# Kernel tuning notes

Measured on AMD Instinct MI355X. Metric: run time of the kernel, lower is better.

Reference implementation:

```python
import jax, jax.numpy as jnp
import numpy as np


def rosa_batch(bits):
    """Vectorized ROSA (suffix-automaton 'predict next symbol of longest previously
    seen suffix') for a batch of binary sequences.

    bits: [N, T] int32 in {0,1}. Returns [N, T] int32 in {-1, 0, 1}.

    Equivalent to the serial suffix-automaton: at step i, let L = max_{j<i}
    lcs(i, j) (longest common suffix of prefixes ending at i and j). If L == 0
    the answer is -1; otherwise let e = max{ j < i : lcs(i, j) == L } (most
    recent occurrence end, matching the automaton's last-endpos bookkeeping)
    and the answer is bits[e + 1]. lcs follows the standard recurrence
    lcs(i, j) = (x[i] == x[j]) * (lcs(i-1, j-1) + 1), computed with a scan
    over i carrying the length-T lcs row, vmapped implicitly over N.
    """
    N, T = bits.shape
    jpos = jnp.arange(T)

    def step(prev, it):
        i, xt = it  # i: scalar step index, xt: [N] current symbols
        # prev[:, j] = lcs(i-1, j); shift to get lcs(i-1, j-1)
        shifted = jnp.concatenate([jnp.zeros((N, 1), prev.dtype), prev[:, :-1]], axis=1)
        cur = jnp.where(bits == xt[:, None], shifted + 1, 0)  # [N, T] lcs(i, j)
        valid = jpos[None, :] < i
        cm = jnp.where(valid, cur, -1)
        L = cm.max(axis=1)  # [N] longest previously-seen suffix length
        # most recent j < i achieving the max
        e = jnp.where(valid & (cm == L[:, None]), jpos[None, :], -1).max(axis=1)
        nxt = jnp.take_along_axis(bits, jnp.clip(e + 1, 0, T - 1)[:, None], axis=1)[:, 0]
        y = jnp.where(L > 0, nxt, -1)
        return cur, y

    _, ys = jax.lax.scan(step, jnp.zeros((N, T), jnp.int32), (jnp.arange(T), bits.T))
    return ys.T


def rosa_bits_btc(bits_btc):
    """bits_btc: [B, T, C] -> idx [B, T, C]; ROSA runs along T per (b, c)."""
    B, T, C = bits_btc.shape
    seqs = bits_btc.transpose(0, 2, 1).reshape(B * C, T)
    return rosa_batch(seqs).reshape(B, C, T).transpose(0, 2, 1)


def setup_inputs() -> dict:
    key = jax.random.key(0)
    B, T, C = 4, 2048, 128
    x = jax.random.normal(key, (B, T, C), dtype=jnp.float32)
    emb0 = jnp.full((1, 1, C), -1e-5, dtype=jnp.float32)
    emb1 = jnp.full((1, 1, C), 1e-5, dtype=jnp.float32)
    return {"x": x, "emb0": emb0, "emb1": emb1}


def reference(x, emb0, emb1):
    bits = (x > 0).astype(jnp.int32)
    idx = rosa_bits_btc(bits)  # [B, T, C] in {-1, 0, 1}
    return jnp.where(idx == -1, jnp.zeros_like(x), jnp.where(idx == 1, emb1, emb0))
```

## Files before the change

kernel.cpp:

```cpp
#include <hip/hip_runtime.h>


#define TT 2048
#define CC 128
#define NW 64
#define NSEQ 512
#define SBITS_WORDS (NSEQ * NW)
#define RES_WORDS (NSEQ * TT)

typedef short          s16x2 __attribute__((ext_vector_type(2)));
typedef unsigned short u16x2 __attribute__((ext_vector_type(2)));

__device__ __forceinline__ unsigned pk_sign(unsigned x) {
    s16x2 v = __builtin_bit_cast(s16x2, x);
    v = v >> 15;
    return __builtin_bit_cast(unsigned, v);
}
__device__ __forceinline__ unsigned pk_shl1(unsigned x) {
    u16x2 v = __builtin_bit_cast(u16x2, x);
    v = v << 1;
    return __builtin_bit_cast(unsigned, v);
}
__device__ __forceinline__ unsigned pk_addsat64(unsigned x) {
    u16x2 v = __builtin_bit_cast(u16x2, x);
    u16x2 c = {64, 64};
    v = __builtin_elementwise_add_sat(v, c);
    return __builtin_bit_cast(unsigned, v);
}
__device__ __forceinline__ unsigned pk_maxu(unsigned a, unsigned b) {
    u16x2 x = __builtin_bit_cast(u16x2, a);
    u16x2 y = __builtin_bit_cast(u16x2, b);
    u16x2 r = __builtin_elementwise_max(x, y);
    return __builtin_bit_cast(unsigned, r);
}

__global__ void k_bits(const float* __restrict__ x, unsigned* __restrict__ sbits)
{
    const int b = blockIdx.x >> 6;
    const int w = blockIdx.x & 63;
    const int t = threadIdx.x;
    __shared__ unsigned char sbyt[32 * 132];

    #pragma unroll
    for (int r = 0; r < 16; ++r) {
        const int e  = t + (r << 8);
        const int ii = e >> 7;
        const int c  = e & 127;
        const float v = x[((size_t)(b * TT + (w << 5) + ii)) * CC + c];
        sbyt[ii * 132 + c] = (v > 0.0f) ? 1u : 0u;
    }
    __syncthreads();

    if (t < CC) {
        unsigned word = 0u;
        #pragma unroll
        for (int ii = 0; ii < 32; ++ii)
            word |= (unsigned)(sbyt[ii * 132 + t] & 1u) << ii;
        sbits[((b << 7) | t) * NW + w] = word;
    }
}

__global__ __launch_bounds__(256, 4) void k_dp2(
    const unsigned* __restrict__ sbits, unsigned* __restrict__ res)
{
    const int u = blockIdx.x;
    const int q = blockIdx.y;
    int k = 0;
    #pragma unroll
    for (int kk = 1; kk < 8; ++kk) if (u >= (kk * (kk + 1)) / 2) k = kk;
    const int chunk = u - (k * (k + 1)) / 2;
    const int D0 = 1 + (chunk << 8);

    const int tid  = threadIdx.x;
    const int lane = tid & 63;
    const int wv   = tid >> 6;
    const int g    = lane >> 3;
    const int lm   = lane & 7;
    const int wB   = k << 3;
    const int wloc = wB + lm;
    const int kb   = k << 8;

    __shared__ unsigned pad[128];
    __shared__ unsigned seedl[256];
    __shared__ unsigned wres[4][8][33];

    if (tid < 64) pad[tid] = 0u;
    else if (tid < 128) pad[tid] = sbits[q * NW + (tid - 64)];
    __syncthreads();

    {
        const int d = D0 + tid;
        unsigned acc = 0u;
        if (d < kb) {
            const int dw = d >> 5, dr = d & 31;
            for (int w = wB - 1; w >= 0; --w) {
                const int sw = w - dw;
                const unsigned u0 = pad[64 + sw];
                const unsigned u1 = pad[63 + sw];
                const unsigned shw = dr ? ((u0 << dr) | (u1 >> (32 - dr))) : u0;
                const unsigned ew = (sw > 0) ? 0xFFFFFFFFu
                                  : ((sw == 0) ? (0xFFFFFFFFu << dr) : 0u);
                const unsigned mw = (~(pad[64 + w] ^ shw)) & ew;
                const unsigned t2 = (mw == 0xFFFFFFFFu) ? 32u
                                  : (unsigned)__builtin_clz(~mw);
                acc += t2;
                if (t2 < 32u) break;
            }
        }
        seedl[tid] = acc;
    }
    __syncthreads();

    const unsigned a = pad[64 + wloc];

    unsigned lmaxp[16];
    #pragma unroll
    for (int j = 0; j < 16; ++j) lmaxp[j] = 0u;

    unsigned incs[8];

    #pragma unroll
    for (int it = 0; it < 8; ++it) {
        const int d  = D0 + (it << 5) + (wv << 3) + g;
        const int dw = d >> 5;
        const int dr = d & 31;

        const int s = wloc - dw;
        const unsigned b0 = pad[64 + s];
        const unsigned b1 = pad[63 + s];
        const unsigned sh = dr ? ((b0 << dr) | (b1 >> (32 - dr))) : b0;
        const unsigned em = (s > 0) ? 0xFFFFFFFFu
                          : ((s == 0) ? (0xFFFFFFFFu << dr) : 0u);
        const unsigned m = (~(a ^ sh)) & em;

        const unsigned seedv = seedl[(it << 5) + (wv << 3) + g];
        const unsigned pm = (unsigned)__shfl_up((int)m, 1, 64);
        const unsigned lead = (unsigned)__builtin_clz(~pm | 1u);
        unsigned inc = (lm == 0) ? seedv : lead;

        if (__builtin_expect(
                __ballot((lm > 0) && (pm == 0xFFFFFFFFu)) != 0ULL, 0)) {
            if ((lm > 0) && (pm == 0xFFFFFFFFu)) {
                unsigned acc = 0u;
                int w;
                for (w = wloc - 1; w >= wB; --w) {
                    const int sw = w - dw;
                    const unsigned u0 = pad[64 + sw];
                    const unsigned u1 = pad[63 + sw];
                    const unsigned shw = dr ? ((u0 << dr) | (u1 >> (32 - dr))) : u0;
                    const unsigned ew = (sw > 0) ? 0xFFFFFFFFu
                                      : ((sw == 0) ? (0xFFFFFFFFu << dr) : 0u);
                    const unsigned mw = (~(pad[64 + w] ^ shw)) & ew;
                    const unsigned t2 = (mw == 0xFFFFFFFFu) ? 32u
                                      : (unsigned)__builtin_clz(~mw);
                    acc += t2;
                    if (t2 < 32u) break;
                }
                if (w < wB) acc += seedv;
                inc = acc;
            }
        }
        incs[it] = inc;

        const unsigned nm   = ~m;
        const unsigned u16c = (unsigned)__builtin_clz((nm << 16) | 0x8000u);
        const unsigned s16  = u16c + ((u16c == 16u) ? inc : 0u);

        const unsigned itcv = (unsigned)((7 - it) << 3) * 0x10001u;
        const unsigned ci = inc > 1023u ? 1023u : inc;
        const unsigned cs = s16 > 1023u ? 1023u : s16;
        unsigned rp = (ci << 6) | (cs << 22) | itcv;

        const unsigned mr  = __builtin_bitreverse32(m);
        unsigned mmr = (mr >> 16) | (mr << 16);

        #pragma unroll
        for (int j = 0; j < 16; ++j) {
            const unsigned sm = pk_sign(mmr);
            mmr = pk_shl1(mmr);
            rp  = pk_addsat64(rp);
            rp  = (rp & sm) | (itcv & ~sm);
            lmaxp[j] = pk_maxu(lmaxp[j], rp);
        }
    }

    const unsigned gk2 = (unsigned)(7 - g) * 0x10001u;
    #pragma unroll
    for (int j = 0; j < 16; ++j) lmaxp[j] |= gk2;

    #pragma unroll
    for (int j = 0; j < 16; ++j) {
        unsigned v = lmaxp[j];
        v = pk_maxu(v, (unsigned)__shfl_xor((int)v, 8, 64));
        v = pk_maxu(v, (unsigned)__shfl_xor((int)v, 16, 64));
        v = pk_maxu(v, (unsigned)__shfl_xor((int)v, 32, 64));
        lmaxp[j] = v;
    }

    unsigned mx = lmaxp[0];
    #pragma unroll
    for (int j = 1; j < 16; ++j) mx = pk_maxu(mx, lmaxp[j]);
    const bool ovf = ((mx & 0x0000FC00u) == 0x0000FC00u) ||
                     ((mx & 0xFC000000u) == 0xFC000000u);

    if (__builtin_expect(__ballot(ovf) == 0ULL, 1)) {
        const unsigned Kw = 2048u - (unsigned)D0 - (unsigned)(wv << 3) - 231u;
        #pragma unroll
        for (int e = 0; e < 4; ++e) {
            const int j = ((g & 3) << 2) + e;
            const unsigned r32 = lmaxp[j];
            const unsigned h = (g >= 4) ? (r32 >> 16) : (r32 & 0xFFFFu);
            const unsigned v = ((h >> 6) << 11) + ((h & 0x38u) << 2) + (h & 7u) + Kw;
            wres[wv][lm][(g << 2) + e] = v;
        }
    } else {
        unsigned lm32[32];
        #pragma unroll
        for (int bb = 0; bb < 32; ++bb) lm32[bb] = 0u;
        for (int it = 0; it < 8; ++it) {
            const int d  = D0 + (it << 5) + (wv << 3) + g;
            const int dw = d >> 5;
            const int dr = d & 31;
            const unsigned dcode = (unsigned)(TT - d) & 2047u;
            const int s = wloc - dw;
            const unsigned b0 = pad[64 + s];
            const unsigned b1 = pad[63 + s];
            const unsigned sh = dr ? ((b0 << dr) | (b1 >> (32 - dr))) : b0;
            const unsigned em = (s > 0) ? 0xFFFFFFFFu
                              : ((s == 0) ? (0xFFFFFFFFu << dr) : 0u);
            const unsigned m = (~(a ^ sh)) & em;
            unsigned pkv = (incs[it] << 11) | dcode;
            for (int bb = 0; bb < 32; ++bb) {
                pkv = ((m >> bb) & 1u) ? (pkv + 0x800u) : dcode;
                lm32[bb] = lm32[bb] >= pkv ? lm32[bb] : pkv;
            }
        }
        #pragma unroll
        for (int bb = 0; bb < 32; ++bb) {
            unsigned v = lm32[bb];
            v = max(v, (unsigned)__shfl_xor((int)v, 8, 64));
            v = max(v, (unsigned)__shfl_xor((int)v, 16, 64));
            v = max(v, (unsigned)__shfl_xor((int)v, 32, 64));
            lm32[bb] = v;
        }
        if (g == 0) {
            #pragma unroll
            for (int bb = 0; bb < 32; ++bb) wres[wv][lm][bb] = lm32[bb];
        }
    }
    __syncthreads();

    {
        const int lw = tid >> 5, bb = tid & 31;
        const unsigned v = max(max(wres[0][lw][bb], wres[1][lw][bb]),
                               max(wres[2][lw][bb], wres[3][lw][bb]));
        if (v >> 11) {
            const int i = ((wB + lw) << 5) + bb;
            atomicMax(&res[(size_t)q * TT + i], v);
        }
    }
}

__global__ void k_dec(const unsigned* __restrict__ sbits,
                      const unsigned* __restrict__ res,
                      const float* __restrict__ emb0,
                      const float* __restrict__ emb1,
                      float* __restrict__ out)
{
    const int b  = blockIdx.y;
    const int i0 = blockIdx.x << 4;
    const int t  = threadIdx.x;
    __shared__ float trans[16][CC + 4];

    const int c  = t >> 1;
    const int q8 = (t & 1) << 3;
    const unsigned* rp = res + ((size_t)((b << 7) | c) * TT) + i0 + q8;
    const unsigned* bw = sbits + ((size_t)((b << 7) | c)) * NW;
    const float e0 = emb0[c], e1 = emb1[c];

    #pragma unroll
    for (int jj = 0; jj < 8; ++jj) {
        const unsigned v = rp[jj];
        const int i = i0 + q8 + jj;
        float val = 0.0f;
        if (v >> 11) {
            const int d   = TT - (int)(v & 2047u);
            const int e1p = i - d + 1;
            val = ((bw[e1p >> 5] >> (e1p & 31)) & 1u) ? e1 : e0;
        }
        trans[q8 + jj][c] = val;
    }
    __syncthreads();

    const int ii = t >> 4;
    const int c0 = (t & 15) << 3;
    float4 w0 = *(const float4*)&trans[ii][c0];
    float4 w1 = *(const float4*)&trans[ii][c0 + 4];
    float* op = out + ((size_t)(b * TT + i0 + ii)) * CC + c0;
    *(float4*)op       = w0;
    *(float4*)(op + 4) = w1;
}

extern "C" void kernel_launch(void* const* d_in, const int* in_sizes, int n_in,
                              void* d_out, int out_size, void* d_ws, size_t ws_size,
                              hipStream_t stream)
{
    const float* x    = (const float*)d_in[0];
    const float* emb0 = (const float*)d_in[1];
    const float* emb1 = (const float*)d_in[2];
    float* out        = (float*)d_out;

    unsigned* sbits = (unsigned*)d_ws;
    unsigned* res   = (unsigned*)d_ws + SBITS_WORDS;

    hipMemsetAsync((void*)res, 0, (size_t)RES_WORDS * 4, stream);
    k_bits<<<dim3(4 * 64), dim3(256), 0, stream>>>(x, sbits);
    k_dp2<<<dim3(36, NSEQ), dim3(256), 0, stream>>>(sbits, res);
    k_dec<<<dim3(TT / 16, 4), dim3(256), 0, stream>>>(sbits, res, emb0, emb1, out);
}
```

Measured before the change: 168.9 us.

## Double diagonal chunk per block to halve DP block count and amortize setup

Each k_dp2 block now covers 512 diagonals (16 iterations) instead of 256, so the grid shrinks from 36 to 20 blocks per sequence. The packed 16-bit max encoding is rebalanced to 4 bits of iteration tag and 9-bit length saturation, with matching changes to the overflow threshold and decode constants. The aim is to amortize per-block setup (pad load, seed computation, reductions, writeback) over more work. In exchange there are fewer blocks for parallelism, more overflow-fallback cases because of the smaller length cap, and the fallback path now recomputes inc instead of storing it.

Measured after the change: 160.4 us. 5.0% less time.

```diff
diff --git a/kernel.cpp b/kernel.cpp
--- a/kernel.cpp
+++ b/kernel.cpp
@@ -21,9 +21,9 @@
     v = v << 1;
     return __builtin_bit_cast(unsigned, v);
 }
-__device__ __forceinline__ unsigned pk_addsat64(unsigned x) {
+__device__ __forceinline__ unsigned pk_addsat128(unsigned x) {
     u16x2 v = __builtin_bit_cast(u16x2, x);
-    u16x2 c = {64, 64};
+    u16x2 c = {128, 128};
     v = __builtin_elementwise_add_sat(v, c);
     return __builtin_bit_cast(unsigned, v);
 }
@@ -66,10 +66,17 @@
     const int u = blockIdx.x;
     const int q = blockIdx.y;
     int k = 0;
-    #pragma unroll
-    for (int kk = 1; kk < 8; ++kk) if (u >= (kk * (kk + 1)) / 2) k = kk;
-    const int chunk = u - (k * (k + 1)) / 2;
-    const int D0 = 1 + (chunk << 8);
+    if (u >= 1)  k = 1;
+    if (u >= 2)  k = 2;
+    if (u >= 4)  k = 3;
+    if (u >= 6)  k = 4;
+    if (u >= 9)  k = 5;
+    if (u >= 12) k = 6;
+    if (u >= 16) k = 7;
+    const int OFFk = (k == 0) ? 0 : (k == 1) ? 1 : (k == 2) ? 2 : (k == 3) ? 4
+                   : (k == 4) ? 6 : (k == 5) ? 9 : (k == 6) ? 12 : 16;
+    const int chunk = u - OFFk;
+    const int D0 = 1 + (chunk << 9);
 
     const int tid  = threadIdx.x;
     const int lane = tid & 63;
@@ -81,15 +88,16 @@
     const int kb   = k << 8;
 
     __shared__ unsigned pad[128];
-    __shared__ unsigned seedl[256];
+    __shared__ unsigned seedl[512];
     __shared__ unsigned wres[4][8][33];
 
     if (tid < 64) pad[tid] = 0u;
     else if (tid < 128) pad[tid] = sbits[q * NW + (tid - 64)];
     __syncthreads();
 
-    {
-        const int d = D0 + tid;
+    #pragma unroll
+    for (int e = 0; e < 2; ++e) {
+        const int d = D0 + tid + (e << 8);
         unsigned acc = 0u;
         if (d < kb) {
             const int dw = d >> 5, dr = d & 31;
@@ -107,7 +115,7 @@
                 if (t2 < 32u) break;
             }
         }
-        seedl[tid] = acc;
+        seedl[tid + (e << 8)] = acc;
     }
     __syncthreads();
 
@@ -117,10 +125,8 @@
     #pragma unroll
     for (int j = 0; j < 16; ++j) lmaxp[j] = 0u;
 
-    unsigned incs[8];
-
-    #pragma unroll
-    for (int it = 0; it < 8; ++it) {
+    #pragma unroll
+    for (int it = 0; it < 16; ++it) {
         const int d  = D0 + (it << 5) + (wv << 3) + g;
         const int dw = d >> 5;
         const int dr = d & 31;
@@ -160,16 +166,15 @@
                 inc = acc;
             }
         }
-        incs[it] = inc;
 
         const unsigned nm   = ~m;
         const unsigned u16c = (unsigned)__builtin_clz((nm << 16) | 0x8000u);
         const unsigned s16  = u16c + ((u16c == 16u) ? inc : 0u);
 
-        const unsigned itcv = (unsigned)((7 - it) << 3) * 0x10001u;
-        const unsigned ci = inc > 1023u ? 1023u : inc;
-        const unsigned cs = s16 > 1023u ? 1023u : s16;
-        unsigned rp = (ci << 6) | (cs << 22) | itcv;
+        const unsigned itcv = (unsigned)((15 - it) << 3) * 0x10001u;
+        const unsigned ci = inc > 511u ? 511u : inc;
+        const unsigned cs = s16 > 511u ? 511u : s16;
+        unsigned rp = (ci << 7) | (cs << 23) | itcv;
 
         const unsigned mr  = __builtin_bitreverse32(m);
         unsigned mmr = (mr >> 16) | (mr << 16);
@@ -178,7 +183,7 @@
         for (int j = 0; j < 16; ++j) {
             const unsigned sm = pk_sign(mmr);
             mmr = pk_shl1(mmr);
-            rp  = pk_addsat64(rp);
+            rp  = pk_addsat128(rp);
             rp  = (rp & sm) | (itcv & ~sm);
             lmaxp[j] = pk_maxu(lmaxp[j], rp);
         }
@@ -200,24 +205,24 @@
     unsigned mx = lmaxp[0];
     #pragma unroll
     for (int j = 1; j < 16; ++j) mx = pk_maxu(mx, lmaxp[j]);
-    const bool ovf = ((mx & 0x0000FC00u) == 0x0000FC00u) ||
-                     ((mx & 0xFC000000u) == 0xFC000000u);
+    const bool ovf = ((mx & 0x0000F000u) == 0x0000F000u) ||
+                     ((mx & 0xF0000000u) == 0xF0000000u);
 
     if (__builtin_expect(__ballot(ovf) == 0ULL, 1)) {
-        const unsigned Kw = 2048u - (unsigned)D0 - (unsigned)(wv << 3) - 231u;
+        const unsigned Kw = 1561u - (unsigned)D0 - (unsigned)(wv << 3);
         #pragma unroll
         for (int e = 0; e < 4; ++e) {
             const int j = ((g & 3) << 2) + e;
             const unsigned r32 = lmaxp[j];
             const unsigned h = (g >= 4) ? (r32 >> 16) : (r32 & 0xFFFFu);
-            const unsigned v = ((h >> 6) << 11) + ((h & 0x38u) << 2) + (h & 7u) + Kw;
+            const unsigned v = ((h >> 7) << 11) + ((h & 0x78u) << 2) + (h & 7u) + Kw;
             wres[wv][lm][(g << 2) + e] = v;
         }
     } else {
         unsigned lm32[32];
         #pragma unroll
         for (int bb = 0; bb < 32; ++bb) lm32[bb] = 0u;
-        for (int it = 0; it < 8; ++it) {
+        for (int it = 0; it < 16; ++it) {
             const int d  = D0 + (it << 5) + (wv << 3) + g;
             const int dw = d >> 5;
             const int dr = d & 31;
@@ -229,7 +234,33 @@
             const unsigned em = (s > 0) ? 0xFFFFFFFFu
                               : ((s == 0) ? (0xFFFFFFFFu << dr) : 0u);
             const unsigned m = (~(a ^ sh)) & em;
-            unsigned pkv = (incs[it] << 11) | dcode;
+
+            const unsigned seedv = seedl[(it << 5) + (wv << 3) + g];
+            const unsigned pm = (unsigned)__shfl_up((int)m, 1, 64);
+            unsigned inc;
+            if (lm == 0) inc = seedv;
+            else if (pm != 0xFFFFFFFFu) inc = (unsigned)__builtin_clz(~pm);
+            else {
+                unsigned acc = 0u;
+                int w;
+                for (w = wloc - 1; w >= wB; --w) {
+                    const int sw = w - dw;
+                    const unsigned u0 = pad[64 + sw];
+                    const unsigned u1 = pad[63 + sw];
+                    const unsigned shw = dr ? ((u0 << dr) | (u1 >> (32 - dr))) : u0;
+                    const unsigned ew = (sw > 0) ? 0xFFFFFFFFu
+                                      : ((sw == 0) ? (0xFFFFFFFFu << dr) : 0u);
+                    const unsigned mw = (~(pad[64 + w] ^ shw)) & ew;
+                    const unsigned t2 = (mw == 0xFFFFFFFFu) ? 32u
+                                      : (unsigned)__builtin_clz(~mw);
+                    acc += t2;
+                    if (t2 < 32u) break;
+                }
+                if (w < wB) acc += seedv;
+                inc = acc;
+            }
+
+            unsigned pkv = (inc << 11) | dcode;
             for (int bb = 0; bb < 32; ++bb) {
                 pkv = ((m >> bb) & 1u) ? (pkv + 0x800u) : dcode;
                 lm32[bb] = lm32[bb] >= pkv ? lm32[bb] : pkv;
@@ -315,6 +346,6 @@
 
     hipMemsetAsync((void*)res, 0, (size_t)RES_WORDS * 4, stream);
     k_bits<<<dim3(4 * 64), dim3(256), 0, stream>>>(x, sbits);
-    k_dp2<<<dim3(36, NSEQ), dim3(256), 0, stream>>>(sbits, res);
+    k_dp2<<<dim3(20, NSEQ), dim3(256), 0, stream>>>(sbits, res);
     k_dec<<<dim3(TT / 16, 4), dim3(256), 0, stream>>>(sbits, res, emb0, emb1, out);
 }
```
